# Kernel optimization log

Measured on AMD Instinct MI355X. Metric: run time of the kernel, lower is better.

## Reference

```python
import jax, jax.numpy as jnp
import numpy as np

B = 8
A = 1614
TOPN = 6
IOU_THR = 0.25
PAD = 224
OUT = 224

def _make_anchors():
    # 6 anchor shapes on the 14x14 map, 6 on 7x7, 9 on 4x4 -> 1614 total,
    # ordered anchor-type-major then row-major spatial to match the [C,H,W] flatten
    # of the tidy conv outputs (as generate_default_anchor_maps does in NTS-Net).
    specs = [
        (14, 32.0, [(48, 48), (64, 48), (48, 64), (80, 80), (96, 64), (64, 96)]),
        (7, 64.0, [(96, 96), (128, 96), (96, 128), (160, 160), (192, 128), (128, 192)]),
        (4, 112.0, [(192, 192), (256, 192), (192, 256), (288, 288), (320, 256), (256, 320), (352, 352), (384, 320), (320, 384)]),
    ]
    blocks = []
    for fm, stride, sizes in specs:
        c = (np.arange(fm) + 0.5) * stride
        cy, cx = np.meshgrid(c, c, indexing='ij')
        for (h, w) in sizes:
            blocks.append(np.stack([cy - h / 2, cx - w / 2, cy + h / 2, cx + w / 2], -1).reshape(-1, 4))
    a = (np.concatenate(blocks, 0) + PAD).astype(np.int64)  # mimic (edge_anchors+224).astype(int)
    return a.astype(np.float32)  # [1614,4] (y0,x0,y1,x1) in padded-image coords

def _conv(x, w, b, stride, pad):
    y = jax.lax.conv_general_dilated(x, w, (stride, stride), [(pad, pad), (pad, pad)],
                                     dimension_numbers=('NCHW', 'OIHW', 'NCHW'))
    return y + b[None, :, None, None]

def _rpn_scores(rpn, wd1, bd1, wd2, bd2, wd3, bd3, wt1, bt1, wt2, bt2, wt3, bt3):
    b = rpn.shape[0]
    d1 = jax.nn.relu(_conv(rpn, wd1, bd1, 1, 1))   # [B,128,14,14]
    d2 = jax.nn.relu(_conv(d1, wd2, bd2, 2, 1))    # [B,128,7,7]
    d3 = jax.nn.relu(_conv(d2, wd3, bd3, 2, 1))    # [B,128,4,4]
    t1 = _conv(d1, wt1, bt1, 1, 0).reshape(b, -1)  # [B,1176]
    t2 = _conv(d2, wt2, bt2, 1, 0).reshape(b, -1)  # [B,294]
    t3 = _conv(d3, wt3, bt3, 1, 0).reshape(b, -1)  # [B,144]
    return jnp.concatenate([t1, t2, t3], axis=1)   # [B,1614]

def _nms_keep(boxes, scores):
    # Greedy NMS over all A anchors; returns keep mask in ORIGINAL anchor order.
    order = jnp.argsort(-scores)
    b = boxes[order]
    y0, x0, y1, x1 = b[:, 0], b[:, 1], b[:, 2], b[:, 3]
    area = (y1 - y0) * (x1 - x0)
    ih = jnp.clip(jnp.minimum(y1[:, None], y1[None, :]) - jnp.maximum(y0[:, None], y0[None, :]), 0)
    iw = jnp.clip(jnp.minimum(x1[:, None], x1[None, :]) - jnp.maximum(x0[:, None], x0[None, :]), 0)
    inter = ih * iw
    iou = inter / (area[:, None] + area[None, :] - inter)
    idx = jnp.arange(A)
    def body(i, supp):
        row = (iou[i] > IOU_THR) & (idx > i)
        return jnp.where(supp[i], supp, supp | row)
    supp = jax.lax.fori_loop(0, A, body, jnp.zeros((A,), bool))
    return jnp.zeros((A,), bool).at[order].set(~supp)

def _crop_resize(img, box):
    # img [3,Hp,Wp]; box int32 (x0,y0,x1,y1).
    # Equivalent to F.interpolate(img[:, y0:y1, x0:x1], (224,224), 'bilinear', align_corners=True)
    x0, y0, x1, y1 = box[0], box[1], box[2], box[3]
    t = jnp.arange(OUT, dtype=jnp.float32) / (OUT - 1)
    sy = y0.astype(jnp.float32) + t * (y1 - 1 - y0).astype(jnp.float32)
    sx = x0.astype(jnp.float32) + t * (x1 - 1 - x0).astype(jnp.float32)
    y0i = jnp.floor(sy).astype(jnp.int32); x0i = jnp.floor(sx).astype(jnp.int32)
    y1i = jnp.minimum(y0i + 1, y1 - 1);    x1i = jnp.minimum(x0i + 1, x1 - 1)
    wy = (sy - y0i.astype(jnp.float32))[None, :, None]
    wx = (sx - x0i.astype(jnp.float32))[None, None, :]
    g = lambda yi, xi: img[:, yi][:, :, xi]  # gather rows then cols -> [3,224,224]
    top = (1 - wx) * g(y0i, x0i) + wx * g(y0i, x1i)
    bot = (1 - wx) * g(y1i, x0i) + wx * g(y1i, x1i)
    return (1 - wy) * top + wy * bot

def setup_inputs():
    key = jax.random.key(0)
    ks = jax.random.split(key, 16)
    n = jax.random.normal
    return {
        'x': n(ks[0], (B, 3, 448, 448), jnp.float32),
        'rpn_feature': n(ks[1], (B, 2048, 14, 14), jnp.float32),
        'anchors': jnp.asarray(_make_anchors()),
        'wd1': 0.02 * n(ks[2], (128, 2048, 3, 3), jnp.float32), 'bd1': 0.01 * n(ks[3], (128,), jnp.float32),
        'wd2': 0.05 * n(ks[4], (128, 128, 3, 3), jnp.float32),  'bd2': 0.01 * n(ks[5], (128,), jnp.float32),
        'wd3': 0.05 * n(ks[6], (128, 128, 3, 3), jnp.float32),  'bd3': 0.01 * n(ks[7], (128,), jnp.float32),
        'wt1': 0.1 * n(ks[8], (6, 128, 1, 1), jnp.float32),     'bt1': 0.01 * n(ks[9], (6,), jnp.float32),
        'wt2': 0.1 * n(ks[10], (6, 128, 1, 1), jnp.float32),    'bt2': 0.01 * n(ks[11], (6,), jnp.float32),
        'wt3': 0.1 * n(ks[12], (9, 128, 1, 1), jnp.float32),    'bt3': 0.01 * n(ks[13], (9,), jnp.float32),
    }

def reference(x, rpn_feature, anchors, wd1, bd1, wd2, bd2, wd3, bd3, wt1, bt1, wt2, bt2, wt3, bt3):
    scores = _rpn_scores(rpn_feature, wd1, bd1, wd2, bd2, wd3, bd3, wt1, bt1, wt2, bt2, wt3, bt3)
    keep = jax.vmap(lambda s: _nms_keep(anchors, s))(scores)           # [B,A] bool
    masked = jnp.where(keep, scores, -jnp.inf)
    top_prob, top_idx = jax.lax.top_k(masked, TOPN)                    # [B,6]
    tb = anchors[top_idx]                                              # [B,6,4] (y0,x0,y1,x1)
    coords = jnp.stack([tb[..., 1], tb[..., 0], tb[..., 3], tb[..., 2]], -1)  # (x0,y0,x1,y1)
    x_pad = jnp.pad(x, ((0, 0), (0, 0), (PAD, PAD), (PAD, PAD)))       # [B,3,896,896]
    bint = coords.astype(jnp.int32)
    part_imgs = jax.vmap(lambda img, bs: jax.vmap(lambda bb: _crop_resize(img, bb))(bs))(x_pad, bint)  # [B,6,3,224,224]
    return part_imgs, coords, top_prob, top_idx
```

## Files before the change

### kernel.cpp

```cpp
#include <hip/hip_runtime.h>
#include <hip/hip_bf16.h>
#include <math.h>
#include <stdint.h>


#define OFF_COORDS 7225344
#define OFF_PROB   7225536
#define OFF_IDX    7225584
#define NA 1614
#define K1TOT 18432

typedef __attribute__((ext_vector_type(8)))  short  short8;
typedef __attribute__((ext_vector_type(16))) float  floatx16;

__global__ __launch_bounds__(256) void k_prep_a(const float* __restrict__ rpn,
                                                __hip_bfloat16* __restrict__ ah,
                                                __hip_bfloat16* __restrict__ al)
{
    __shared__ float tile[64][65];
    const int cib  = blockIdx.x * 64;
    const int posb = blockIdx.y * 64;
    const int b    = blockIdx.z;
    const int t    = threadIdx.x;
#pragma unroll
    for (int it = 0; it < 16; ++it) {
        int idx  = it * 256 + t;
        int cil  = idx >> 6;
        int posl = idx & 63;
        int pos  = posb + posl;
        int py = pos >> 4, px = pos & 15;
        int y = py - 1, x = px - 1;
        float v = 0.0f;
        if ((unsigned)y < 14u && (unsigned)x < 14u)
            v = rpn[((size_t)(b * 2048 + cib + cil) * 14 + y) * 14 + x];
        tile[cil][posl] = v;
    }
    __syncthreads();
#pragma unroll
    for (int it = 0; it < 16; ++it) {
        int idx  = it * 256 + t;
        int posl = idx >> 6;
        int cil  = idx & 63;
        float v = tile[cil][posl];
        __hip_bfloat16 h = __float2bfloat16(v);
        __hip_bfloat16 l = __float2bfloat16(v - __bfloat162float(h));
        size_t o = (size_t)(b * 256 + posb + posl) * 2048 + cib + cil;
        ah[o] = h; al[o] = l;
    }
}

__global__ __launch_bounds__(256) void k_prep_b(const float* __restrict__ w,
                                                __hip_bfloat16* __restrict__ bh,
                                                __hip_bfloat16* __restrict__ bl)
{
    const int tap = blockIdx.x;
    const int co  = blockIdx.y;
    const int t   = threadIdx.x;
#pragma unroll
    for (int i = 0; i < 8; ++i) {
        int ci = i * 256 + t;
        float v = w[((size_t)co * 2048 + ci) * 9 + tap];
        __hip_bfloat16 h = __float2bfloat16(v);
        __hip_bfloat16 l = __float2bfloat16(v - __bfloat162float(h));
        size_t o = (size_t)co * K1TOT + tap * 2048 + ci;
        bh[o] = h; bl[o] = l;
    }
}

__global__ __launch_bounds__(256) void k_conv1_mfma(const short* __restrict__ ah,
                                                    const short* __restrict__ al,
                                                    const short* __restrict__ bh,
                                                    const short* __restrict__ bl,
                                                    float* __restrict__ partial,
                                                    int chunk)
{
    __shared__ short AsH[128][40];
    __shared__ short AsL[128][40];
    __shared__ short BsH[128][40];
    __shared__ short BsL[128][40];

    const int t     = threadIdx.x;
    const int lane  = t & 63;
    const int w     = t >> 6;
    const int wm    = (w & 1) * 64;
    const int wn    = (w >> 1) * 64;
    const int lm    = lane & 31;
    const int half  = lane >> 5;
    const int mbase = blockIdx.x * 128;
    const int k0    = blockIdx.y * chunk;
    const int k1    = (k0 + chunk < K1TOT) ? (k0 + chunk) : K1TOT;

    int arow[2], apos[2]; bool aval[2];
    const int akc = (t & 3) * 8;
#pragma unroll
    for (int i = 0; i < 2; ++i) {
        int row = ((i * 256 + t) >> 2);
        int m   = mbase + row;
        arow[i] = row;
        aval[i] = (m < 1568);
        int mm = aval[i] ? m : 0;
        int b  = mm / 196;
        int p  = mm - b * 196;
        int y  = p / 14;
        int x  = p - y * 14;
        apos[i] = b * 256 + y * 16 + x;
    }

    floatx16 acc[2][2];
#pragma unroll
    for (int mf = 0; mf < 2; ++mf)
#pragma unroll
        for (int nf = 0; nf < 2; ++nf)
#pragma unroll
            for (int r = 0; r < 16; ++r) acc[mf][nf][r] = 0.0f;

    const short8 zero8 = {0, 0, 0, 0, 0, 0, 0, 0};

    for (int ks = k0; ks < k1; ks += 32) {
        const int tap = ks >> 11;
        const int ci0 = ks & 2047;
        const int dy  = tap / 3, dx = tap - dy * 3;
#pragma unroll
        for (int i = 0; i < 2; ++i) {
            short8 vh = zero8, vl = zero8;
            if (aval[i]) {
                size_t g = (size_t)(apos[i] + dy * 16 + dx) * 2048 + ci0 + akc;
                vh = *(const short8*)(ah + g);
                vl = *(const short8*)(al + g);
            }
            *(short8*)&AsH[arow[i]][akc] = vh;
            *(short8*)&AsL[arow[i]][akc] = vl;
        }
#pragma unroll
        for (int i = 0; i < 2; ++i) {
            int n = ((i * 256 + t) >> 2);
            size_t g = (size_t)n * K1TOT + ks + akc;
            *(short8*)&BsH[n][akc] = *(const short8*)(bh + g);
            *(short8*)&BsL[n][akc] = *(const short8*)(bl + g);
        }
        __syncthreads();
#pragma unroll
        for (int kst = 0; kst < 2; ++kst) {
            const int koff = kst * 16 + half * 8;
            short8 a_h[2], a_l[2], b_h[2], b_l[2];
#pragma unroll
            for (int mf = 0; mf < 2; ++mf) {
                a_h[mf] = *(const short8*)&AsH[wm + mf * 32 + lm][koff];
                a_l[mf] = *(const short8*)&AsL[wm + mf * 32 + lm][koff];
            }
#pragma unroll
            for (int nf = 0; nf < 2; ++nf) {
                b_h[nf] = *(const short8*)&BsH[wn + nf * 32 + lm][koff];
                b_l[nf] = *(const short8*)&BsL[wn + nf * 32 + lm][koff];
            }
#pragma unroll
            for (int mf = 0; mf < 2; ++mf)
#pragma unroll
                for (int nf = 0; nf < 2; ++nf) {
                    acc[mf][nf] = __builtin_amdgcn_mfma_f32_32x32x16_bf16(
                        a_h[mf], b_h[nf], acc[mf][nf], 0, 0, 0);
                    acc[mf][nf] = __builtin_amdgcn_mfma_f32_32x32x16_bf16(
                        a_h[mf], b_l[nf], acc[mf][nf], 0, 0, 0);
                    acc[mf][nf] = __builtin_amdgcn_mfma_f32_32x32x16_bf16(
                        a_l[mf], b_h[nf], acc[mf][nf], 0, 0, 0);
                }
        }
        __syncthreads();
    }

    float* P = partial + (size_t)blockIdx.y * 1568 * 128;
#pragma unroll
    for (int mf = 0; mf < 2; ++mf)
#pragma unroll
        for (int nf = 0; nf < 2; ++nf)
#pragma unroll
            for (int r = 0; r < 16; ++r) {
                int row = (r & 3) + 8 * (r >> 2) + 4 * half;
                int m = mbase + wm + mf * 32 + row;
                int n = wn + nf * 32 + lm;
                if (m < 1568) P[(size_t)m * 128 + n] = acc[mf][nf][r];
            }
}

__global__ __launch_bounds__(256) void k_transpose_w(const float* __restrict__ w,
                                                     float* __restrict__ wt, int K)
{
    __shared__ float tile[32][33];
    int kb = blockIdx.x * 32;
    int cb = blockIdx.y * 32;
    int tx = threadIdx.x;
    int ty = threadIdx.y;
#pragma unroll
    for (int j = 0; j < 32; j += 8) {
        int co = cb + ty + j;
        int k  = kb + tx;
        tile[ty + j][tx] = (k < K) ? w[(size_t)co * K + k] : 0.0f;
    }
    __syncthreads();
#pragma unroll
    for (int j = 0; j < 32; j += 8) {
        int k  = kb + ty + j;
        int co = cb + tx;
        if (k < K) wt[(size_t)k * 128 + co] = tile[tx][ty + j];
    }
}

template<int CIN, int HIN, int WIN, int HOUT, int WOUT, int STR>
__global__ __launch_bounds__(256) void k_conv_gemm(const float* __restrict__ in,
                                                   const float* __restrict__ wt,
                                                   float* __restrict__ partial,
                                                   int kchunk)
{
    constexpr int PSZ  = HOUT * WOUT;
    constexpr int M    = 8 * PSZ;
    constexpr int KTOT = CIN * 9;
    __shared__ float As[16][64];
    __shared__ float Bs[16][128];
    const int t  = threadIdx.x;
    const int tx = t & 15;
    const int ty = t >> 4;
    const int mbase = blockIdx.x * 64;
    const int k0 = blockIdx.y * kchunk;
    const int k1 = (k0 + kchunk < KTOT) ? (k0 + kchunk) : KTOT;

    float acc[4][8];
#pragma unroll
    for (int r = 0; r < 4; ++r)
#pragma unroll
        for (int c = 0; c < 8; ++c) acc[r][c] = 0.0f;

    for (int ks = k0; ks < k1; ks += 16) {
#pragma unroll
        for (int i = 0; i < 4; ++i) {
            int e  = i * 256 + t;
            int kk = e >> 6;
            int mm = e & 63;
            int k  = ks + kk;
            int m  = mbase + mm;
            float v = 0.0f;
            if (k < k1 && m < M) {
                int ci  = k / 9;
                int tap = k - ci * 9;
                int b = m / PSZ;
                int p = m - b * PSZ;
                int y = p / WOUT;
                int x = p - y * WOUT;
                int yy = y * STR + tap / 3 - 1;
                int xx = x * STR + (tap % 3) - 1;
                if (yy >= 0 && yy < HIN && xx >= 0 && xx < WIN)
                    v = in[(((size_t)b * CIN + ci) * HIN + yy) * WIN + xx];
            }
            As[kk][mm] = v;
        }
#pragma unroll
        for (int i = 0; i < 8; ++i) {
            int e  = i * 256 + t;
            int kk = e >> 7;
            int co = e & 127;
            int k  = ks + kk;
            Bs[kk][co] = (k < k1) ? wt[(size_t)k * 128 + co] : 0.0f;
        }
        __syncthreads();
#pragma unroll
        for (int kk = 0; kk < 16; ++kk) {
            float a[4], bb[8];
            *(float4*)&a[0]  = *(const float4*)&As[kk][ty * 4];
            *(float4*)&bb[0] = *(const float4*)&Bs[kk][tx * 8];
            *(float4*)&bb[4] = *(const float4*)&Bs[kk][tx * 8 + 4];
#pragma unroll
            for (int r = 0; r < 4; ++r)
#pragma unroll
                for (int c = 0; c < 8; ++c)
                    acc[r][c] = fmaf(a[r], bb[c], acc[r][c]);
        }
        __syncthreads();
    }

    float* P = partial + (size_t)blockIdx.y * M * 128;
#pragma unroll
    for (int r = 0; r < 4; ++r) {
        int m = mbase + ty * 4 + r;
        if (m < M) {
            *(float4*)&P[(size_t)m * 128 + tx * 8]     = *(const float4*)&acc[r][0];
            *(float4*)&P[(size_t)m * 128 + tx * 8 + 4] = *(const float4*)&acc[r][4];
        }
    }
}

template<int PSZ>
__global__ __launch_bounds__(256) void k_reduce_bias(const float* __restrict__ partial,
                                                     const float* __restrict__ bias,
                                                     float* __restrict__ out,
                                                     int ksplit, int relu)
{
    constexpr int M = 8 * PSZ;
    int idx = blockIdx.x * 256 + threadIdx.x;
    if (idx >= M * 128) return;
    int m  = idx >> 7;
    int co = idx & 127;
    float s = bias[co];
    for (int k = 0; k < ksplit; ++k) s += partial[(size_t)k * M * 128 + idx];
    if (relu) s = fmaxf(s, 0.0f);
    int b = m / PSZ;
    int p = m - b * PSZ;
    out[((size_t)b * 128 + co) * PSZ + p] = s;
}

__global__ __launch_bounds__(256) void k_heads(const float* __restrict__ d1,
                                               const float* __restrict__ d2,
                                               const float* __restrict__ d3,
                                               const float* __restrict__ w1, const float* __restrict__ b1,
                                               const float* __restrict__ w2, const float* __restrict__ b2,
                                               const float* __restrict__ w3, const float* __restrict__ b3,
                                               float* __restrict__ scores)
{
    int idx = blockIdx.x * 256 + threadIdx.x;
    if (idx >= 8 * NA) return;
    int b = idx / NA;
    int e = idx - b * NA;
    const float* d; const float* w; float bias; int psz;
    if (e < 1176) {
        int c = e / 196, p = e - c * 196;
        d = d1 + (size_t)b * 128 * 196 + p; w = w1 + c * 128; bias = b1[c]; psz = 196;
    } else if (e < 1470) {
        int e2 = e - 1176; int c = e2 / 49, p = e2 - c * 49;
        d = d2 + (size_t)b * 128 * 49 + p; w = w2 + c * 128; bias = b2[c]; psz = 49;
    } else {
        int e2 = e - 1470; int c = e2 / 16, p = e2 - c * 16;
        d = d3 + (size_t)b * 128 * 16 + p; w = w3 + c * 128; bias = b3[c]; psz = 16;
    }
    float s = bias;
    const float* dp = d;
    for (int ci = 0; ci < 128; ++ci) { s = fmaf(*dp, w[ci], s); dp += psz; }
    scores[idx] = s;
}

__global__ __launch_bounds__(256) void k_nms_topk(const float* __restrict__ scores,
                                                  const float* __restrict__ anchors,
                                                  float* __restrict__ out,
                                                  int* __restrict__ boxes)
{
    __shared__ float ms[NA];
    __shared__ float ay0[NA], ax0[NA], ay1[NA], ax1[NA];
    __shared__ unsigned char picked[NA];
    __shared__ float rv[4]; __shared__ int ri[4];
    __shared__ float win[5];
    int b = blockIdx.x;
    int t = threadIdx.x;
    for (int i = t; i < NA; i += 256) {
        ms[i] = scores[b * NA + i];
        float4 an = ((const float4*)anchors)[i];
        ay0[i] = an.x; ax0[i] = an.y; ay1[i] = an.z; ax1[i] = an.w;
        picked[i] = 0;
    }
    __syncthreads();
    for (int r = 0; r < 6; ++r) {
        float bv = -INFINITY; int bi = NA;
        for (int i = t; i < NA; i += 256) {
            if (!picked[i]) {
                float v = ms[i];
                if (v > bv || (v == bv && i < bi)) { bv = v; bi = i; }
            }
        }
#pragma unroll
        for (int off = 32; off > 0; off >>= 1) {
            float v2 = __shfl_down(bv, off);
            int   i2 = __shfl_down(bi, off);
            if (v2 > bv || (v2 == bv && i2 < bi)) { bv = v2; bi = i2; }
        }
        if ((t & 63) == 0) { rv[t >> 6] = bv; ri[t >> 6] = bi; }
        __syncthreads();
        if (t == 0) {
            bv = rv[0]; bi = ri[0];
            for (int wv = 1; wv < 4; ++wv)
                if (rv[wv] > bv || (rv[wv] == bv && ri[wv] < bi)) { bv = rv[wv]; bi = ri[wv]; }
            picked[bi] = 1;
            win[0] = ay0[bi]; win[1] = ax0[bi]; win[2] = ay1[bi]; win[3] = ax1[bi]; win[4] = bv;
            int o = b * 6 + r;
            out[OFF_COORDS + o * 4 + 0] = ax0[bi];
            out[OFF_COORDS + o * 4 + 1] = ay0[bi];
            out[OFF_COORDS + o * 4 + 2] = ax1[bi];
            out[OFF_COORDS + o * 4 + 3] = ay1[bi];
            out[OFF_PROB + o] = bv;
            out[OFF_IDX  + o] = (float)bi;
            boxes[o * 4 + 0] = (int)ax0[bi];
            boxes[o * 4 + 1] = (int)ay0[bi];
            boxes[o * 4 + 2] = (int)ax1[bi];
            boxes[o * 4 + 3] = (int)ay1[bi];
        }
        __syncthreads();
        float by0 = win[0], bx0 = win[1], by1 = win[2], bx1 = win[3];
        float barea = (by1 - by0) * (bx1 - bx0);
        for (int i = t; i < NA; i += 256) {
            if (picked[i]) continue;
            float ih = fmaxf(fminf(by1, ay1[i]) - fmaxf(by0, ay0[i]), 0.0f);
            float iw = fmaxf(fminf(bx1, ax1[i]) - fmaxf(bx0, ax0[i]), 0.0f);
            float inter = ih * iw;
            float area  = (ay1[i] - ay0[i]) * (ax1[i] - ax0[i]);
            float iou = inter / (barea + area - inter);
            if (iou > 0.25f) ms[i] = -INFINITY;
        }
        __syncthreads();
    }
}

__global__ __launch_bounds__(256) void k_crop(const float* __restrict__ x,
                                              const int* __restrict__ boxes,
                                              float* __restrict__ out)
{
    int bid = blockIdx.x;
    int i = threadIdx.x;
    if (i >= 224) return;
    int j   = bid % 224;
    int rem = bid / 224;
    int c   = rem % 3;
    int br  = rem / 3;
    int b   = br / 6;
    int4 bx = ((const int4*)boxes)[br];
    float tj = (float)j / 223.0f;
    float sy = (float)bx.y + tj * (float)(bx.w - 1 - bx.y);
    int y0i = (int)floorf(sy);
    int y1i = min(y0i + 1, bx.w - 1);
    float wy = sy - (float)y0i;
    float ti = (float)i / 223.0f;
    float sx = (float)bx.x + ti * (float)(bx.z - 1 - bx.x);
    int x0i = (int)floorf(sx);
    int x1i = min(x0i + 1, bx.z - 1);
    float wx = sx - (float)x0i;
    const float* img = x + ((size_t)b * 3 + c) * 448 * 448;
    auto g = [&](int yy, int xx) -> float {
        yy -= 224; xx -= 224;
        if ((unsigned)yy >= 448u || (unsigned)xx >= 448u) return 0.0f;
        return img[(size_t)yy * 448 + xx];
    };
    float g00 = g(y0i, x0i), g01 = g(y0i, x1i);
    float g10 = g(y1i, x0i), g11 = g(y1i, x1i);
    float top = (1.0f - wx) * g00 + wx * g01;
    float bot = (1.0f - wx) * g10 + wx * g11;
    out[(size_t)bid * 224 + i] = (1.0f - wy) * top + wy * bot;
}

extern "C" void kernel_launch(void* const* d_in, const int* in_sizes, int n_in,
                              void* d_out, int out_size, void* d_ws, size_t ws_size,
                              hipStream_t stream)
{
    (void)in_sizes; (void)n_in; (void)out_size;
    const float* x    = (const float*)d_in[0];
    const float* rpn  = (const float*)d_in[1];
    const float* anch = (const float*)d_in[2];
    const float* wd1  = (const float*)d_in[3];
    const float* bd1  = (const float*)d_in[4];
    const float* wd2  = (const float*)d_in[5];
    const float* bd2  = (const float*)d_in[6];
    const float* wd3  = (const float*)d_in[7];
    const float* bd3  = (const float*)d_in[8];
    const float* hw1  = (const float*)d_in[9];
    const float* hb1  = (const float*)d_in[10];
    const float* hw2  = (const float*)d_in[11];
    const float* hb2  = (const float*)d_in[12];
    const float* hw3  = (const float*)d_in[13];
    const float* hb3  = (const float*)d_in[14];
    float* out = (float*)d_out;

    char* ws = (char*)d_ws;
    size_t off = 0;
    auto alloc = [&](size_t bytes) -> void* {
        void* p = ws + off;
        off = (off + bytes + 255) & ~(size_t)255;
        return p;
    };
    __hip_bfloat16* ahb = (__hip_bfloat16*)alloc((size_t)8 * 256 * 2048 * 2);
    __hip_bfloat16* alb = (__hip_bfloat16*)alloc((size_t)8 * 256 * 2048 * 2);
    __hip_bfloat16* bhb = (__hip_bfloat16*)alloc((size_t)128 * K1TOT * 2);
    __hip_bfloat16* blb = (__hip_bfloat16*)alloc((size_t)128 * K1TOT * 2);
    float* tw2   = (float*)alloc((size_t)1152 * 128 * 4);
    float* tw3   = (float*)alloc((size_t)1152 * 128 * 4);
    float* d1    = (float*)alloc((size_t)8 * 128 * 196 * 4);
    float* d2    = (float*)alloc((size_t)8 * 128 * 49 * 4);
    float* d3    = (float*)alloc((size_t)8 * 128 * 16 * 4);
    float* sc    = (float*)alloc((size_t)8 * NA * 4);
    int*   boxes = (int*)alloc((size_t)8 * 6 * 4 * 4);
    size_t avail = (ws_size > off) ? (ws_size - off) : 0;
    float* P = (float*)(ws + off);

    long long s1 = (long long)(avail / ((size_t)1568 * 128 * 4));
    if (s1 > 48) s1 = 48;
    if (s1 < 1)  s1 = 1;
    int S1 = (int)s1;
    int chunk1 = ((K1TOT + S1 * 32 - 1) / (S1 * 32)) * 32;

    auto pick_ksplit = [&](int M) -> int {
        size_t per = (size_t)M * 128 * 4;
        long long ks = (per > 0) ? (long long)(avail / per) : 1;
        if (ks > 16) ks = 16;
        if (ks < 1)  ks = 1;
        return (int)ks;
    };

    k_prep_a<<<dim3(32, 4, 8), 256, 0, stream>>>(rpn, ahb, alb);
    k_prep_b<<<dim3(9, 128), 256, 0, stream>>>(wd1, bhb, blb);
    k_conv1_mfma<<<dim3(13, S1), 256, 0, stream>>>((const short*)ahb, (const short*)alb,
                                                   (const short*)bhb, (const short*)blb,
                                                   P, chunk1);
    k_reduce_bias<196><<<dim3((1568 * 128 + 255) / 256), 256, 0, stream>>>(P, bd1, d1, S1, 1);

    dim3 tb(32, 8);
    k_transpose_w<<<dim3(36, 4), tb, 0, stream>>>(wd2, tw2, 1152);
    k_transpose_w<<<dim3(36, 4), tb, 0, stream>>>(wd3, tw3, 1152);

    int ks2 = pick_ksplit(392);
    int kc2 = (1152 + ks2 - 1) / ks2;
    k_conv_gemm<128, 14, 14, 7, 7, 2><<<dim3(7, ks2), 256, 0, stream>>>(d1, tw2, P, kc2);
    k_reduce_bias<49><<<dim3((392 * 128 + 255) / 256), 256, 0, stream>>>(P, bd2, d2, ks2, 1);

    int ks3 = pick_ksplit(128);
    int kc3 = (1152 + ks3 - 1) / ks3;
    k_conv_gemm<128, 7, 7, 4, 4, 2><<<dim3(2, ks3), 256, 0, stream>>>(d2, tw3, P, kc3);
    k_reduce_bias<16><<<dim3((128 * 128 + 255) / 256), 256, 0, stream>>>(P, bd3, d3, ks3, 1);

    k_heads<<<dim3((8 * NA + 255) / 256), 256, 0, stream>>>(d1, d2, d3, hw1, hb1, hw2, hb2, hw3, hb3, sc);
    k_nms_topk<<<dim3(8), 256, 0, stream>>>(sc, anch, out, boxes);
    k_crop<<<dim3(8 * 6 * 3 * 224), 256, 0, stream>>>(x, boxes, out);
}
```

Baseline: 291.8 us.

## Run conv2/conv3 on split-bf16 MFMA with padded NHWC activations

Templates the conv1 MFMA kernel so it handles conv2 and conv3 too, replacing the scalar fp32 tiled GEMM kernels. The reduce step now writes zero-padded NHWC hi/lo bf16 copies for the next MFMA conv. It also writes NHWC fp32 activations, and the heads kernel reads those with float4 vector dot products. This removes the weight transposes and the slow fp32 GEMMs, at the cost of extra prep launches and a bf16x3 approximation of fp32 accuracy.

```diff
diff --git a/kernel.cpp b/kernel.cpp
--- a/kernel.cpp
+++ b/kernel.cpp
@@ -67,13 +67,36 @@
     }
 }
 
-__global__ __launch_bounds__(256) void k_conv1_mfma(const short* __restrict__ ah,
-                                                    const short* __restrict__ al,
-                                                    const short* __restrict__ bh,
-                                                    const short* __restrict__ bl,
-                                                    float* __restrict__ partial,
-                                                    int chunk)
-{
+__global__ __launch_bounds__(128) void k_prep_w23(const float* __restrict__ w2,
+                                                  const float* __restrict__ w3,
+                                                  __hip_bfloat16* __restrict__ b2h,
+                                                  __hip_bfloat16* __restrict__ b2l,
+                                                  __hip_bfloat16* __restrict__ b3h,
+                                                  __hip_bfloat16* __restrict__ b3l)
+{
+    const int tap = blockIdx.x;
+    const int co  = blockIdx.y;
+    const int z   = blockIdx.z;
+    const int ci  = threadIdx.x;
+    const float* w = z ? w3 : w2;
+    __hip_bfloat16* bh = z ? b3h : b2h;
+    __hip_bfloat16* bl = z ? b3l : b2l;
+    float v = w[((size_t)co * 128 + ci) * 9 + tap];
+    __hip_bfloat16 h = __float2bfloat16(v);
+    __hip_bfloat16 l = __float2bfloat16(v - __bfloat162float(h));
+    size_t o = (size_t)co * 1152 + tap * 128 + ci;
+    bh[o] = h; bl[o] = l;
+}
+
+template<int POSN, int OW, int STR, int CIN, int MTOT>
+__global__ __launch_bounds__(256) void k_conv_mfma(const short* __restrict__ ah,
+                                                   const short* __restrict__ al,
+                                                   const short* __restrict__ bh,
+                                                   const short* __restrict__ bl,
+                                                   float* __restrict__ partial,
+                                                   int chunk)
+{
+    constexpr int KTOT = CIN * 9;
     __shared__ short AsH[128][40];
     __shared__ short AsL[128][40];
     __shared__ short BsH[128][40];
@@ -88,7 +111,7 @@
     const int half  = lane >> 5;
     const int mbase = blockIdx.x * 128;
     const int k0    = blockIdx.y * chunk;
-    const int k1    = (k0 + chunk < K1TOT) ? (k0 + chunk) : K1TOT;
+    const int k1    = (k0 + chunk < KTOT) ? (k0 + chunk) : KTOT;
 
     int arow[2], apos[2]; bool aval[2];
     const int akc = (t & 3) * 8;
@@ -97,13 +120,13 @@
         int row = ((i * 256 + t) >> 2);
         int m   = mbase + row;
         arow[i] = row;
-        aval[i] = (m < 1568);
+        aval[i] = (m < MTOT);
         int mm = aval[i] ? m : 0;
-        int b  = mm / 196;
-        int p  = mm - b * 196;
-        int y  = p / 14;
-        int x  = p - y * 14;
-        apos[i] = b * 256 + y * 16 + x;
+        int b  = mm / POSN;
+        int p  = mm - b * POSN;
+        int y  = p / OW;
+        int x  = p - y * OW;
+        apos[i] = b * 256 + y * STR * 16 + x * STR;
     }
 
     floatx16 acc[2][2];
@@ -117,14 +140,14 @@
     const short8 zero8 = {0, 0, 0, 0, 0, 0, 0, 0};
 
     for (int ks = k0; ks < k1; ks += 32) {
-        const int tap = ks >> 11;
-        const int ci0 = ks & 2047;
+        const int tap = ks / CIN;
+        const int ci0 = ks - tap * CIN;
         const int dy  = tap / 3, dx = tap - dy * 3;
 #pragma unroll
         for (int i = 0; i < 2; ++i) {
             short8 vh = zero8, vl = zero8;
             if (aval[i]) {
-                size_t g = (size_t)(apos[i] + dy * 16 + dx) * 2048 + ci0 + akc;
+                size_t g = (size_t)(apos[i] + dy * 16 + dx) * CIN + ci0 + akc;
                 vh = *(const short8*)(ah + g);
                 vl = *(const short8*)(al + g);
             }
@@ -134,7 +157,7 @@
 #pragma unroll
         for (int i = 0; i < 2; ++i) {
             int n = ((i * 256 + t) >> 2);
-            size_t g = (size_t)n * K1TOT + ks + akc;
+            size_t g = (size_t)n * KTOT + ks + akc;
             *(short8*)&BsH[n][akc] = *(const short8*)(bh + g);
             *(short8*)&BsL[n][akc] = *(const short8*)(bl + g);
         }
@@ -168,7 +191,7 @@
         __syncthreads();
     }
 
-    float* P = partial + (size_t)blockIdx.y * 1568 * 128;
+    float* P = partial + (size_t)blockIdx.y * MTOT * 128;
 #pragma unroll
     for (int mf = 0; mf < 2; ++mf)
 #pragma unroll
@@ -178,137 +201,54 @@
                 int row = (r & 3) + 8 * (r >> 2) + 4 * half;
                 int m = mbase + wm + mf * 32 + row;
                 int n = wn + nf * 32 + lm;
-                if (m < 1568) P[(size_t)m * 128 + n] = acc[mf][nf][r];
+                if (m < MTOT) P[(size_t)m * 128 + n] = acc[mf][nf][r];
             }
 }
 
-__global__ __launch_bounds__(256) void k_transpose_w(const float* __restrict__ w,
-                                                     float* __restrict__ wt, int K)
-{
-    __shared__ float tile[32][33];
-    int kb = blockIdx.x * 32;
-    int cb = blockIdx.y * 32;
-    int tx = threadIdx.x;
-    int ty = threadIdx.y;
-#pragma unroll
-    for (int j = 0; j < 32; j += 8) {
-        int co = cb + ty + j;
-        int k  = kb + tx;
-        tile[ty + j][tx] = (k < K) ? w[(size_t)co * K + k] : 0.0f;
-    }
-    __syncthreads();
-#pragma unroll
-    for (int j = 0; j < 32; j += 8) {
-        int k  = kb + ty + j;
-        int co = cb + tx;
-        if (k < K) wt[(size_t)k * 128 + co] = tile[tx][ty + j];
-    }
-}
-
-template<int CIN, int HIN, int WIN, int HOUT, int WOUT, int STR>
-__global__ __launch_bounds__(256) void k_conv_gemm(const float* __restrict__ in,
-                                                   const float* __restrict__ wt,
-                                                   float* __restrict__ partial,
-                                                   int kchunk)
-{
-    constexpr int PSZ  = HOUT * WOUT;
-    constexpr int M    = 8 * PSZ;
-    constexpr int KTOT = CIN * 9;
-    __shared__ float As[16][64];
-    __shared__ float Bs[16][128];
-    const int t  = threadIdx.x;
-    const int tx = t & 15;
-    const int ty = t >> 4;
-    const int mbase = blockIdx.x * 64;
-    const int k0 = blockIdx.y * kchunk;
-    const int k1 = (k0 + kchunk < KTOT) ? (k0 + kchunk) : KTOT;
-
-    float acc[4][8];
-#pragma unroll
-    for (int r = 0; r < 4; ++r)
-#pragma unroll
-        for (int c = 0; c < 8; ++c) acc[r][c] = 0.0f;
-
-    for (int ks = k0; ks < k1; ks += 16) {
-#pragma unroll
-        for (int i = 0; i < 4; ++i) {
-            int e  = i * 256 + t;
-            int kk = e >> 6;
-            int mm = e & 63;
-            int k  = ks + kk;
-            int m  = mbase + mm;
-            float v = 0.0f;
-            if (k < k1 && m < M) {
-                int ci  = k / 9;
-                int tap = k - ci * 9;
-                int b = m / PSZ;
-                int p = m - b * PSZ;
-                int y = p / WOUT;
-                int x = p - y * WOUT;
-                int yy = y * STR + tap / 3 - 1;
-                int xx = x * STR + (tap % 3) - 1;
-                if (yy >= 0 && yy < HIN && xx >= 0 && xx < WIN)
-                    v = in[(((size_t)b * CIN + ci) * HIN + yy) * WIN + xx];
-            }
-            As[kk][mm] = v;
-        }
-#pragma unroll
-        for (int i = 0; i < 8; ++i) {
-            int e  = i * 256 + t;
-            int kk = e >> 7;
-            int co = e & 127;
-            int k  = ks + kk;
-            Bs[kk][co] = (k < k1) ? wt[(size_t)k * 128 + co] : 0.0f;
-        }
-        __syncthreads();
-#pragma unroll
-        for (int kk = 0; kk < 16; ++kk) {
-            float a[4], bb[8];
-            *(float4*)&a[0]  = *(const float4*)&As[kk][ty * 4];
-            *(float4*)&bb[0] = *(const float4*)&Bs[kk][tx * 8];
-            *(float4*)&bb[4] = *(const float4*)&Bs[kk][tx * 8 + 4];
-#pragma unroll
-            for (int r = 0; r < 4; ++r)
-#pragma unroll
-                for (int c = 0; c < 8; ++c)
-                    acc[r][c] = fmaf(a[r], bb[c], acc[r][c]);
-        }
-        __syncthreads();
-    }
-
-    float* P = partial + (size_t)blockIdx.y * M * 128;
-#pragma unroll
-    for (int r = 0; r < 4; ++r) {
-        int m = mbase + ty * 4 + r;
-        if (m < M) {
-            *(float4*)&P[(size_t)m * 128 + tx * 8]     = *(const float4*)&acc[r][0];
-            *(float4*)&P[(size_t)m * 128 + tx * 8 + 4] = *(const float4*)&acc[r][4];
-        }
-    }
-}
-
-template<int PSZ>
-__global__ __launch_bounds__(256) void k_reduce_bias(const float* __restrict__ partial,
-                                                     const float* __restrict__ bias,
-                                                     float* __restrict__ out,
-                                                     int ksplit, int relu)
-{
-    constexpr int M = 8 * PSZ;
+template<int POSN, int OWV>
+__global__ __launch_bounds__(256) void k_reduce_pad(const float* __restrict__ partial,
+                                                    const float* __restrict__ bias,
+                                                    float* __restrict__ dn,
+                                                    __hip_bfloat16* __restrict__ ph,
+                                                    __hip_bfloat16* __restrict__ pl,
+                                                    int S)
+{
+    constexpr int MTOT = 8 * POSN;
     int idx = blockIdx.x * 256 + threadIdx.x;
-    if (idx >= M * 128) return;
-    int m  = idx >> 7;
-    int co = idx & 127;
+    int b   = idx >> 15;
+    int pos = (idx >> 7) & 255;
+    int co  = idx & 127;
+    int y = (pos >> 4) - 1;
+    int x = (pos & 15) - 1;
+    if ((unsigned)y < (unsigned)OWV && (unsigned)x < (unsigned)OWV) {
+        int m = b * POSN + y * OWV + x;
+        float s = bias[co];
+        for (int k = 0; k < S; ++k) s += partial[(size_t)k * MTOT * 128 + m * 128 + co];
+        s = fmaxf(s, 0.0f);
+        dn[(size_t)m * 128 + co] = s;
+        __hip_bfloat16 h = __float2bfloat16(s);
+        __hip_bfloat16 l = __float2bfloat16(s - __bfloat162float(h));
+        ph[idx] = h; pl[idx] = l;
+    } else {
+        ph[idx] = __float2bfloat16(0.0f);
+        pl[idx] = __float2bfloat16(0.0f);
+    }
+}
+
+__global__ __launch_bounds__(256) void k_reduce3(const float* __restrict__ partial,
+                                                 const float* __restrict__ bias,
+                                                 float* __restrict__ dn, int S)
+{
+    int idx = blockIdx.x * 256 + threadIdx.x;
+    int co  = idx & 127;
     float s = bias[co];
-    for (int k = 0; k < ksplit; ++k) s += partial[(size_t)k * M * 128 + idx];
-    if (relu) s = fmaxf(s, 0.0f);
-    int b = m / PSZ;
-    int p = m - b * PSZ;
-    out[((size_t)b * 128 + co) * PSZ + p] = s;
-}
-
-__global__ __launch_bounds__(256) void k_heads(const float* __restrict__ d1,
-                                               const float* __restrict__ d2,
-                                               const float* __restrict__ d3,
+    for (int k = 0; k < S; ++k) s += partial[(size_t)k * 128 * 128 + idx];
+    dn[idx] = fmaxf(s, 0.0f);
+}
+
+__global__ __launch_bounds__(256) void k_heads(const float* __restrict__ d1n,
+                                               const float* __restrict__ d2n,
+                                               const float* __restrict__ d3n,
                                                const float* __restrict__ w1, const float* __restrict__ b1,
                                                const float* __restrict__ w2, const float* __restrict__ b2,
                                                const float* __restrict__ w3, const float* __restrict__ b3,
@@ -318,20 +258,27 @@
     if (idx >= 8 * NA) return;
     int b = idx / NA;
     int e = idx - b * NA;
-    const float* d; const float* w; float bias; int psz;
+    const float* d; const float* w; float bias;
     if (e < 1176) {
         int c = e / 196, p = e - c * 196;
-        d = d1 + (size_t)b * 128 * 196 + p; w = w1 + c * 128; bias = b1[c]; psz = 196;
+        d = d1n + (size_t)(b * 196 + p) * 128; w = w1 + c * 128; bias = b1[c];
     } else if (e < 1470) {
         int e2 = e - 1176; int c = e2 / 49, p = e2 - c * 49;
-        d = d2 + (size_t)b * 128 * 49 + p; w = w2 + c * 128; bias = b2[c]; psz = 49;
+        d = d2n + (size_t)(b * 49 + p) * 128; w = w2 + c * 128; bias = b2[c];
     } else {
         int e2 = e - 1470; int c = e2 / 16, p = e2 - c * 16;
-        d = d3 + (size_t)b * 128 * 16 + p; w = w3 + c * 128; bias = b3[c]; psz = 16;
+        d = d3n + (size_t)(b * 16 + p) * 128; w = w3 + c * 128; bias = b3[c];
     }
     float s = bias;
-    const float* dp = d;
-    for (int ci = 0; ci < 128; ++ci) { s = fmaf(*dp, w[ci], s); dp += psz; }
+#pragma unroll
+    for (int i = 0; i < 32; ++i) {
+        float4 dv = ((const float4*)d)[i];
+        float4 wv = ((const float4*)w)[i];
+        s = fmaf(dv.x, wv.x, s);
+        s = fmaf(dv.y, wv.y, s);
+        s = fmaf(dv.z, wv.z, s);
+        s = fmaf(dv.w, wv.w, s);
+    }
     scores[idx] = s;
 }
 
@@ -469,17 +416,23 @@
         off = (off + bytes + 255) & ~(size_t)255;
         return p;
     };
-    __hip_bfloat16* ahb = (__hip_bfloat16*)alloc((size_t)8 * 256 * 2048 * 2);
-    __hip_bfloat16* alb = (__hip_bfloat16*)alloc((size_t)8 * 256 * 2048 * 2);
-    __hip_bfloat16* bhb = (__hip_bfloat16*)alloc((size_t)128 * K1TOT * 2);
-    __hip_bfloat16* blb = (__hip_bfloat16*)alloc((size_t)128 * K1TOT * 2);
-    float* tw2   = (float*)alloc((size_t)1152 * 128 * 4);
-    float* tw3   = (float*)alloc((size_t)1152 * 128 * 4);
-    float* d1    = (float*)alloc((size_t)8 * 128 * 196 * 4);
-    float* d2    = (float*)alloc((size_t)8 * 128 * 49 * 4);
-    float* d3    = (float*)alloc((size_t)8 * 128 * 16 * 4);
-    float* sc    = (float*)alloc((size_t)8 * NA * 4);
-    int*   boxes = (int*)alloc((size_t)8 * 6 * 4 * 4);
+    __hip_bfloat16* ahb  = (__hip_bfloat16*)alloc((size_t)8 * 256 * 2048 * 2);
+    __hip_bfloat16* alb  = (__hip_bfloat16*)alloc((size_t)8 * 256 * 2048 * 2);
+    __hip_bfloat16* b1h  = (__hip_bfloat16*)alloc((size_t)128 * K1TOT * 2);
+    __hip_bfloat16* b1l  = (__hip_bfloat16*)alloc((size_t)128 * K1TOT * 2);
+    __hip_bfloat16* b2h  = (__hip_bfloat16*)alloc((size_t)128 * 1152 * 2);
+    __hip_bfloat16* b2l  = (__hip_bfloat16*)alloc((size_t)128 * 1152 * 2);
+    __hip_bfloat16* b3h  = (__hip_bfloat16*)alloc((size_t)128 * 1152 * 2);
+    __hip_bfloat16* b3l  = (__hip_bfloat16*)alloc((size_t)128 * 1152 * 2);
+    __hip_bfloat16* d1ph = (__hip_bfloat16*)alloc((size_t)8 * 256 * 128 * 2);
+    __hip_bfloat16* d1pl = (__hip_bfloat16*)alloc((size_t)8 * 256 * 128 * 2);
+    __hip_bfloat16* d2ph = (__hip_bfloat16*)alloc((size_t)8 * 256 * 128 * 2);
+    __hip_bfloat16* d2pl = (__hip_bfloat16*)alloc((size_t)8 * 256 * 128 * 2);
+    float* d1n  = (float*)alloc((size_t)8 * 196 * 128 * 4);
+    float* d2n  = (float*)alloc((size_t)8 * 49 * 128 * 4);
+    float* d3n  = (float*)alloc((size_t)8 * 16 * 128 * 4);
+    float* sc   = (float*)alloc((size_t)8 * NA * 4);
+    int*  boxes = (int*)alloc((size_t)8 * 6 * 4 * 4);
     size_t avail = (ws_size > off) ? (ws_size - off) : 0;
     float* P = (float*)(ws + off);
 
@@ -489,36 +442,24 @@
     int S1 = (int)s1;
     int chunk1 = ((K1TOT + S1 * 32 - 1) / (S1 * 32)) * 32;
 
-    auto pick_ksplit = [&](int M) -> int {
-        size_t per = (size_t)M * 128 * 4;
-        long long ks = (per > 0) ? (long long)(avail / per) : 1;
-        if (ks > 16) ks = 16;
-        if (ks < 1)  ks = 1;
-        return (int)ks;
-    };
-
+    k_prep_b<<<dim3(9, 128), 256, 0, stream>>>(wd1, b1h, b1l);
+    k_prep_w23<<<dim3(9, 128, 2), 128, 0, stream>>>(wd2, wd3, b2h, b2l, b3h, b3l);
     k_prep_a<<<dim3(32, 4, 8), 256, 0, stream>>>(rpn, ahb, alb);
-    k_prep_b<<<dim3(9, 128), 256, 0, stream>>>(wd1, bhb, blb);
-    k_conv1_mfma<<<dim3(13, S1), 256, 0, stream>>>((const short*)ahb, (const short*)alb,
-                                                   (const short*)bhb, (const short*)blb,
-                                                   P, chunk1);
-    k_reduce_bias<196><<<dim3((1568 * 128 + 255) / 256), 256, 0, stream>>>(P, bd1, d1, S1, 1);
-
-    dim3 tb(32, 8);
-    k_transpose_w<<<dim3(36, 4), tb, 0, stream>>>(wd2, tw2, 1152);
-    k_transpose_w<<<dim3(36, 4), tb, 0, stream>>>(wd3, tw3, 1152);
-
-    int ks2 = pick_ksplit(392);
-    int kc2 = (1152 + ks2 - 1) / ks2;
-    k_conv_gemm<128, 14, 14, 7, 7, 2><<<dim3(7, ks2), 256, 0, stream>>>(d1, tw2, P, kc2);
-    k_reduce_bias<49><<<dim3((392 * 128 + 255) / 256), 256, 0, stream>>>(P, bd2, d2, ks2, 1);
-
-    int ks3 = pick_ksplit(128);
-    int kc3 = (1152 + ks3 - 1) / ks3;
-    k_conv_gemm<128, 7, 7, 4, 4, 2><<<dim3(2, ks3), 256, 0, stream>>>(d2, tw3, P, kc3);
-    k_reduce_bias<16><<<dim3((128 * 128 + 255) / 256), 256, 0, stream>>>(P, bd3, d3, ks3, 1);
-
-    k_heads<<<dim3((8 * NA + 255) / 256), 256, 0, stream>>>(d1, d2, d3, hw1, hb1, hw2, hb2, hw3, hb3, sc);
+
+    k_conv_mfma<196, 14, 1, 2048, 1568><<<dim3(13, S1), 256, 0, stream>>>(
+        (const short*)ahb, (const short*)alb, (const short*)b1h, (const short*)b1l, P, chunk1);
+    k_reduce_pad<196, 14><<<dim3(1024), 256, 0, stream>>>(P, bd1, d1n, d1ph, d1pl, S1);
+
+    k_conv_mfma<49, 7, 2, 128, 392><<<dim3(4, 9), 256, 0, stream>>>(
+        (const short*)d1ph, (const short*)d1pl, (const short*)b2h, (const short*)b2l, P, 128);
+    k_reduce_pad<49, 7><<<dim3(1024), 256, 0, stream>>>(P, bd2, d2n, d2ph, d2pl, 9);
+
+    k_conv_mfma<16, 4, 2, 128, 128><<<dim3(1, 9), 256, 0, stream>>>(
+        (const short*)d2ph, (const short*)d2pl, (const short*)b3h, (const short*)b3l, P, 128);
+    k_reduce3<<<dim3(64), 256, 0, stream>>>(P, bd3, d3n, 9);
+
+    k_heads<<<dim3((8 * NA + 255) / 256), 256, 0, stream>>>(d1n, d2n, d3n,
+        hw1, hb1, hw2, hb2, hw3, hb3, sc);
     k_nms_topk<<<dim3(8), 256, 0, stream>>>(sc, anch, out, boxes);
     k_crop<<<dim3(8 * 6 * 3 * 224), 256, 0, stream>>>(x, boxes, out);
 }
```

After: 259.1 us. -11.2%, faster.
